# Kernel tuning notes

Hardware: AMD Instinct MI355X
Metric: run time of the kernel (lower is better)

The kernel has to match this reference:

```python
import jax, jax.numpy as jnp
import numpy as np

EPSILON = 1e-8
DAMPING = 0.7
B, PREV, SIZE, NXT = 8192, 2000, 2000, 2000


def standardize(x):
    # per-sample standardization over features (torch.std uses ddof=1)
    mean = x.mean(axis=1, keepdims=True)
    std = jnp.std(x, axis=1, ddof=1, keepdims=True)
    return (x - mean) / (std + EPSILON)


def setup_inputs() -> dict:
    key = jax.random.key(0)
    ks = jax.random.split(key, 9)
    return {
        "prev_act": jax.random.normal(ks[0], (B, PREV), jnp.float32),
        "self_act": jax.random.normal(ks[1], (B, SIZE), jnp.float32),
        "next_act": jax.random.normal(ks[2], (B, NXT), jnp.float32),
        "forward_W": jax.random.normal(ks[3], (SIZE, PREV), jnp.float32) * 0.02,
        "forward_b": jax.random.normal(ks[4], (SIZE,), jnp.float32) * 0.02,
        "backward_W": jax.random.normal(ks[5], (SIZE, NXT), jnp.float32) * 0.02,
        "backward_b": jax.random.normal(ks[6], (SIZE,), jnp.float32) * 0.02,
        "lateral_W": jax.random.normal(ks[7], (SIZE, SIZE), jnp.float32) * 0.02,
        "lateral_b": jax.random.normal(ks[8], (SIZE,), jnp.float32) * 0.02,
    }


def reference(prev_act, self_act, next_act, forward_W, forward_b,
              backward_W, backward_b, lateral_W, lateral_b):
    # middle HiddenLayer forward: fwd(prev) + next.backward(next) + lateral(self)
    prev_s = standardize(prev_act)   # [B, PREV]
    next_s = standardize(next_act)   # [B, NXT]
    self_s = standardize(self_act)   # [B, SIZE]
    pre = (jnp.einsum('bp,sp->bs', prev_s, forward_W) + forward_b
           + jnp.einsum('bn,sn->bs', next_s, backward_W) + backward_b
           + jnp.einsum('bk,sk->bs', self_s, lateral_W) + lateral_b)
    new_act = jax.nn.relu(pre)
    # damped recurrent update
    return DAMPING * new_act + (1.0 - DAMPING) * self_act
```

## Files before the change

kernel.cpp:

```cpp
#include <hip/hip_runtime.h>
#include <hip/hip_bf16.h>

constexpr int BATCH = 8192;
constexpr int NREAL = 2000;
constexpr int KSLOT = 2048;
constexpr int KPAD  = 6144;
constexpr int NPAD  = 2048;
constexpr int NT    = KPAD / 64;

typedef short bf16x8 __attribute__((ext_vector_type(8)));
typedef float f32x4  __attribute__((ext_vector_type(4)));

__device__ inline void gload_lds16(const void* g, void* l) {
  __builtin_amdgcn_global_load_lds(
      (const __attribute__((address_space(1))) unsigned int*)g,
      (__attribute__((address_space(3))) unsigned int*)l,
      16, 0, 0);
}

__device__ inline unsigned short f2bf(float x) {
  union { float f; unsigned int u; } v;
  v.f = x;
  unsigned int r = v.u + 0x7fffu + ((v.u >> 16) & 1u);
  return (unsigned short)(r >> 16);
}

__global__ __launch_bounds__(256) void pack_kernel(
    const float* __restrict__ prev, const float* __restrict__ nxt,
    const float* __restrict__ selfa,
    const float* __restrict__ fW, const float* __restrict__ bW,
    const float* __restrict__ lW,
    unsigned short* __restrict__ Acat, unsigned short* __restrict__ Wcat) {
  const int mat = blockIdx.y;
  const int t = threadIdx.x;

  if (blockIdx.x >= BATCH) {
    const int s = blockIdx.x - BATCH;
    uint4 q = make_uint4(0, 0, 0, 0);
    if (s < NREAL && t < 250) {
      const float* src = ((mat == 0) ? fW : (mat == 1) ? bW : lW) +
                         (size_t)s * NREAL + t * 8;
      const float4* p = (const float4*)src;
      float4 a = p[0], b = p[1];
      q.x = (unsigned)f2bf(a.x) | ((unsigned)f2bf(a.y) << 16);
      q.y = (unsigned)f2bf(a.z) | ((unsigned)f2bf(a.w) << 16);
      q.z = (unsigned)f2bf(b.x) | ((unsigned)f2bf(b.y) << 16);
      q.w = (unsigned)f2bf(b.z) | ((unsigned)f2bf(b.w) << 16);
    }
    *(uint4*)(Wcat + (size_t)s * KPAD + mat * KSLOT + t * 8) = q;
    return;
  }

  __shared__ float red[4];
  const int row = blockIdx.x;
  const float* src = (mat == 0) ? prev : (mat == 1) ? nxt : selfa;

  float x[8];
  float s1 = 0.f;
  if (t < 250) {
    const float4* p = (const float4*)(src + (size_t)row * NREAL + t * 8);
    float4 a = p[0], b = p[1];
    x[0] = a.x; x[1] = a.y; x[2] = a.z; x[3] = a.w;
    x[4] = b.x; x[5] = b.y; x[6] = b.z; x[7] = b.w;
#pragma unroll
    for (int j = 0; j < 8; ++j) s1 += x[j];
  } else {
#pragma unroll
    for (int j = 0; j < 8; ++j) x[j] = 0.f;
  }
#pragma unroll
  for (int o = 32; o; o >>= 1) s1 += __shfl_xor(s1, o);
  if ((t & 63) == 0) red[t >> 6] = s1;
  __syncthreads();
  const float mean = (red[0] + red[1] + red[2] + red[3]) * (1.f / 2000.f);
  __syncthreads();

  float ss = 0.f;
  if (t < 250) {
#pragma unroll
    for (int j = 0; j < 8; ++j) { float d = x[j] - mean; ss += d * d; }
  }
#pragma unroll
  for (int o = 32; o; o >>= 1) ss += __shfl_xor(ss, o);
  if ((t & 63) == 0) red[t >> 6] = ss;
  __syncthreads();
  const float var = (red[0] + red[1] + red[2] + red[3]) * (1.f / 1999.f);
  const float scale = 1.f / (sqrtf(var) + 1e-8f);

  unsigned short o8[8];
  if (t < 250) {
#pragma unroll
    for (int j = 0; j < 8; ++j) o8[j] = f2bf((x[j] - mean) * scale);
  } else {
#pragma unroll
    for (int j = 0; j < 8; ++j) o8[j] = 0;
  }
  uint4 q;
  q.x = (unsigned)o8[0] | ((unsigned)o8[1] << 16);
  q.y = (unsigned)o8[2] | ((unsigned)o8[3] << 16);
  q.z = (unsigned)o8[4] | ((unsigned)o8[5] << 16);
  q.w = (unsigned)o8[6] | ((unsigned)o8[7] << 16);
  *(uint4*)(Acat + (size_t)row * KPAD + mat * KSLOT + t * 8) = q;
}

__global__ __launch_bounds__(512, 2) void gemm_kernel(
    const unsigned short* __restrict__ A,
    const unsigned short* __restrict__ W,
    const float* __restrict__ fb, const float* __restrict__ bb,
    const float* __restrict__ lb,
    const float* __restrict__ selfact,
    float* __restrict__ out) {
  __shared__ unsigned short ldsS[2][2][2][256][32];
  unsigned short* ldsF = &ldsS[0][0][0][0][0];

  const int tid  = threadIdx.x;
  const int wave = tid >> 6;
  const int lane = tid & 63;
  const int wm = wave >> 2;
  const int wn = wave & 3;

  const int nbid = (blockIdx.x & 7) * 32 + (blockIdx.x >> 3);
  const int bm = nbid >> 3;
  const int bn = nbid & 7;

  const int srow = tid >> 2;
  const int sc = (tid & 3) ^ ((tid >> 3) & 3);
  const unsigned short* Asrc =
      A + (size_t)(bm * 256 + srow) * KPAD + sc * 8;
  const unsigned short* Bsrc =
      W + (size_t)(bn * 256 + srow) * KPAD + sc * 8;

  const int pcx = (lane >> 4) ^ ((lane >> 1) & 3);
  const unsigned short* aF = ldsF + (wm * 128 + (lane & 15)) * 32 + pcx * 8;
  const unsigned short* bF = ldsF + (wn * 64 + (lane & 15)) * 32 + pcx * 8;

  f32x4 acc[8][4] = {};
  bf16x8 bfr[4][2];

#define STQ(bu, mat, kq, rh, tt) { \
    const unsigned short* g_ = ((mat) ? Bsrc : Asrc) + \
        (size_t)(rh) * 128 * KPAD + (size_t)(tt) * 64 + (kq) * 32; \
    unsigned short* d_ = ldsF + ((bu) * 4 + (mat) * 2 + (kq)) * 8192 + \
        (rh) * 4096 + wave * 512; \
    gload_lds16(g_, d_); \
  }

#define READ_BF(bu) \
    _Pragma("unroll") for (int fn = 0; fn < 4; ++fn) \
    _Pragma("unroll") for (int kk = 0; kk < 2; ++kk) \
      bfr[fn][kk] = *(const bf16x8*)(bF + ((bu) * 4 + 2 + kk) * 8192 + fn * 512);

#define PHASE(bu, p, STG, GATE) { \
    bf16x8 a00 = *(const bf16x8*)(aF + ((bu) * 4 + 0) * 8192 + (2 * (p)) * 512); \
    bf16x8 a01 = *(const bf16x8*)(aF + ((bu) * 4 + 1) * 8192 + (2 * (p)) * 512); \
    bf16x8 a10 = *(const bf16x8*)(aF + ((bu) * 4 + 0) * 8192 + (2 * (p) + 1) * 512); \
    bf16x8 a11 = *(const bf16x8*)(aF + ((bu) * 4 + 1) * 8192 + (2 * (p) + 1) * 512); \
    if ((p) == 0) { READ_BF(bu) } \
    STG \
    if ((p) == 0) asm volatile("s_waitcnt lgkmcnt(8)" ::: "memory"); \
    __builtin_amdgcn_s_barrier(); \
    asm volatile("s_waitcnt lgkmcnt(0)" ::: "memory"); \
    __builtin_amdgcn_s_setprio(1); \
    _Pragma("unroll") for (int fn = 0; fn < 4; ++fn) { \
      acc[2 * (p)][fn] = __builtin_amdgcn_mfma_f32_16x16x32_bf16( \
          a00, bfr[fn][0], acc[2 * (p)][fn], 0, 0, 0); \
      acc[2 * (p)][fn] = __builtin_amdgcn_mfma_f32_16x16x32_bf16( \
          a01, bfr[fn][1], acc[2 * (p)][fn], 0, 0, 0); \
      acc[2 * (p) + 1][fn] = __builtin_amdgcn_mfma_f32_16x16x32_bf16( \
          a10, bfr[fn][0], acc[2 * (p) + 1][fn], 0, 0, 0); \
      acc[2 * (p) + 1][fn] = __builtin_amdgcn_mfma_f32_16x16x32_bf16( \
          a11, bfr[fn][1], acc[2 * (p) + 1][fn], 0, 0, 0); \
    } \
    __builtin_amdgcn_s_setprio(0); \
    GATE \
    __builtin_amdgcn_s_barrier(); \
  }

#define TILE(bu, t, SA, SB, GATE) { \
    PHASE(bu, 0, if (SA) { STQ((bu) ^ 1, 0, 0, 0, (t) + 1) STQ((bu) ^ 1, 0, 1, 0, (t) + 1) }, ) \
    PHASE(bu, 1, if (SA) { STQ((bu) ^ 1, 0, 0, 1, (t) + 1) STQ((bu) ^ 1, 0, 1, 1, (t) + 1) }, ) \
    PHASE(bu, 2, if (SB) { STQ((bu), 1, 0, 0, (t) + 2) STQ((bu), 1, 1, 0, (t) + 2) }, ) \
    PHASE(bu, 3, if (SB) { STQ((bu), 1, 0, 1, (t) + 2) STQ((bu), 1, 1, 1, (t) + 2) }, GATE) \
  }

  STQ(0, 0, 0, 0, 0) STQ(0, 0, 1, 0, 0)
  STQ(0, 0, 0, 1, 0) STQ(0, 0, 1, 1, 0)
  STQ(0, 1, 0, 0, 0) STQ(0, 1, 1, 0, 0)
  STQ(0, 1, 0, 1, 0) STQ(0, 1, 1, 1, 0)
  STQ(1, 1, 0, 0, 1) STQ(1, 1, 1, 0, 1)
  STQ(1, 1, 0, 1, 1) STQ(1, 1, 1, 1, 1)
  asm volatile("s_waitcnt vmcnt(4)" ::: "memory");
  __builtin_amdgcn_s_barrier();

  for (int i = 0; i < 47; ++i) {
    const int t = 2 * i;
    TILE(0, t, true, true,
         asm volatile("s_waitcnt vmcnt(4)" ::: "memory");)
    TILE(1, t + 1, true, true,
         asm volatile("s_waitcnt vmcnt(4)" ::: "memory");)
  }
  TILE(0, 94, true, false,
       asm volatile("s_waitcnt vmcnt(0)" ::: "memory");)
  TILE(1, 95, false, false, )

  const int colLane = lane & 15;
  const int rowGrp  = (lane >> 4) * 4;
#pragma unroll
  for (int fn = 0; fn < 4; ++fn) {
    const int col = bn * 256 + wn * 64 + fn * 16 + colLane;
    if (col < NREAL) {
      const float bias = fb[col] + bb[col] + lb[col];
#pragma unroll
      for (int fm = 0; fm < 8; ++fm) {
        const int row0 = bm * 256 + wm * 128 + fm * 16 + rowGrp;
#pragma unroll
        for (int r = 0; r < 4; ++r) {
          const float pre = acc[fm][fn][r] + bias;
          const size_t oi = (size_t)(row0 + r) * NREAL + col;
          out[oi] = 0.7f * fmaxf(pre, 0.f) + 0.3f * selfact[oi];
        }
      }
    }
  }
#undef TILE
#undef PHASE
#undef READ_BF
#undef STQ
}

extern "C" void kernel_launch(void* const* d_in, const int* in_sizes, int n_in,
                              void* d_out, int out_size, void* d_ws,
                              size_t ws_size, hipStream_t stream) {
  const float* prev = (const float*)d_in[0];
  const float* selfa = (const float*)d_in[1];
  const float* nxt  = (const float*)d_in[2];
  const float* fW = (const float*)d_in[3];
  const float* fb = (const float*)d_in[4];
  const float* bW = (const float*)d_in[5];
  const float* bb = (const float*)d_in[6];
  const float* lW = (const float*)d_in[7];
  const float* lb = (const float*)d_in[8];
  float* out = (float*)d_out;

  unsigned short* Acat = (unsigned short*)d_ws;
  unsigned short* Wcat = Acat + (size_t)BATCH * KPAD;

  pack_kernel<<<dim3(BATCH + NPAD, 3), 256, 0, stream>>>(
      prev, nxt, selfa, fW, bW, lW, Acat, Wcat);
  gemm_kernel<<<dim3(32 * 8), 512, 0, stream>>>(Acat, Wcat, fb, bb, lb,
                                                selfa, out);
}
```

Baseline: 255.5 us.

## Switch GEMM to 32x32x16 MFMA with simpler double-buffered tile loop

Replaces the 16x16x32 MFMA tiling with 32x32x16 MFMA, so each wave uses 4x2 accumulator blocks of 16 floats and fewer LDS fragment reads per FLOP. It also drops the finely phased four-stage pipeline with partial vmcnt gates. In its place is a plain loop that prefetches the whole next tile, computes the current one, then waits vmcnt(0) and hits a barrier once per tile. The larger MFMA should cut LDS traffic and instruction count, but the coarser synchronisation may expose more global-load latency.

```diff
diff --git a/kernel.cpp b/kernel.cpp
--- a/kernel.cpp
+++ b/kernel.cpp
@@ -9,7 +9,7 @@
 constexpr int NT    = KPAD / 64;
 
 typedef short bf16x8 __attribute__((ext_vector_type(8)));
-typedef float f32x4  __attribute__((ext_vector_type(4)));
+typedef float f32x16 __attribute__((ext_vector_type(16)));
 
 __device__ inline void gload_lds16(const void* g, void* l) {
   __builtin_amdgcn_global_load_lds(
@@ -130,12 +130,21 @@
   const unsigned short* Bsrc =
       W + (size_t)(bn * 256 + srow) * KPAD + sc * 8;
 
-  const int pcx = (lane >> 4) ^ ((lane >> 1) & 3);
-  const unsigned short* aF = ldsF + (wm * 128 + (lane & 15)) * 32 + pcx * 8;
-  const unsigned short* bF = ldsF + (wn * 64 + (lane & 15)) * 32 + pcx * 8;
-
-  f32x4 acc[8][4] = {};
-  bf16x8 bfr[4][2];
+  const int h = lane >> 5;
+  const int l31 = lane & 31;
+  int aOff[4], bOff[2];
+#pragma unroll
+  for (int rg = 0; rg < 4; ++rg) {
+    const int row = wm * 128 + rg * 32 + l31;
+    aOff[rg] = row * 32 + ((h ^ ((row >> 1) & 3)) << 3);
+  }
+#pragma unroll
+  for (int cg = 0; cg < 2; ++cg) {
+    const int row = wn * 64 + cg * 32 + l31;
+    bOff[cg] = row * 32 + ((h ^ ((row >> 1) & 3)) << 3);
+  }
+
+  f32x16 acc[4][2] = {};
 
 #define STQ(bu, mat, kq, rh, tt) { \
     const unsigned short* g_ = ((mat) ? Bsrc : Asrc) + \
@@ -144,87 +153,68 @@
         (rh) * 4096 + wave * 512; \
     gload_lds16(g_, d_); \
   }
-
-#define READ_BF(bu) \
-    _Pragma("unroll") for (int fn = 0; fn < 4; ++fn) \
-    _Pragma("unroll") for (int kk = 0; kk < 2; ++kk) \
-      bfr[fn][kk] = *(const bf16x8*)(bF + ((bu) * 4 + 2 + kk) * 8192 + fn * 512);
-
-#define PHASE(bu, p, STG, GATE) { \
-    bf16x8 a00 = *(const bf16x8*)(aF + ((bu) * 4 + 0) * 8192 + (2 * (p)) * 512); \
-    bf16x8 a01 = *(const bf16x8*)(aF + ((bu) * 4 + 1) * 8192 + (2 * (p)) * 512); \
-    bf16x8 a10 = *(const bf16x8*)(aF + ((bu) * 4 + 0) * 8192 + (2 * (p) + 1) * 512); \
-    bf16x8 a11 = *(const bf16x8*)(aF + ((bu) * 4 + 1) * 8192 + (2 * (p) + 1) * 512); \
-    if ((p) == 0) { READ_BF(bu) } \
-    STG \
-    if ((p) == 0) asm volatile("s_waitcnt lgkmcnt(8)" ::: "memory"); \
-    __builtin_amdgcn_s_barrier(); \
-    asm volatile("s_waitcnt lgkmcnt(0)" ::: "memory"); \
-    __builtin_amdgcn_s_setprio(1); \
-    _Pragma("unroll") for (int fn = 0; fn < 4; ++fn) { \
-      acc[2 * (p)][fn] = __builtin_amdgcn_mfma_f32_16x16x32_bf16( \
-          a00, bfr[fn][0], acc[2 * (p)][fn], 0, 0, 0); \
-      acc[2 * (p)][fn] = __builtin_amdgcn_mfma_f32_16x16x32_bf16( \
-          a01, bfr[fn][1], acc[2 * (p)][fn], 0, 0, 0); \
-      acc[2 * (p) + 1][fn] = __builtin_amdgcn_mfma_f32_16x16x32_bf16( \
-          a10, bfr[fn][0], acc[2 * (p) + 1][fn], 0, 0, 0); \
-      acc[2 * (p) + 1][fn] = __builtin_amdgcn_mfma_f32_16x16x32_bf16( \
-          a11, bfr[fn][1], acc[2 * (p) + 1][fn], 0, 0, 0); \
-    } \
-    __builtin_amdgcn_s_setprio(0); \
-    GATE \
-    __builtin_amdgcn_s_barrier(); \
-  }
-
-#define TILE(bu, t, SA, SB, GATE) { \
-    PHASE(bu, 0, if (SA) { STQ((bu) ^ 1, 0, 0, 0, (t) + 1) STQ((bu) ^ 1, 0, 1, 0, (t) + 1) }, ) \
-    PHASE(bu, 1, if (SA) { STQ((bu) ^ 1, 0, 0, 1, (t) + 1) STQ((bu) ^ 1, 0, 1, 1, (t) + 1) }, ) \
-    PHASE(bu, 2, if (SB) { STQ((bu), 1, 0, 0, (t) + 2) STQ((bu), 1, 1, 0, (t) + 2) }, ) \
-    PHASE(bu, 3, if (SB) { STQ((bu), 1, 0, 1, (t) + 2) STQ((bu), 1, 1, 1, (t) + 2) }, GATE) \
-  }
-
-  STQ(0, 0, 0, 0, 0) STQ(0, 0, 1, 0, 0)
-  STQ(0, 0, 0, 1, 0) STQ(0, 0, 1, 1, 0)
-  STQ(0, 1, 0, 0, 0) STQ(0, 1, 1, 0, 0)
-  STQ(0, 1, 0, 1, 0) STQ(0, 1, 1, 1, 0)
-  STQ(1, 1, 0, 0, 1) STQ(1, 1, 1, 0, 1)
-  STQ(1, 1, 0, 1, 1) STQ(1, 1, 1, 1, 1)
-  asm volatile("s_waitcnt vmcnt(4)" ::: "memory");
+#define STAGE_TILE(bu, tt) { \
+    STQ(bu, 0, 0, 0, tt) STQ(bu, 0, 1, 0, tt) \
+    STQ(bu, 0, 0, 1, tt) STQ(bu, 0, 1, 1, tt) \
+    STQ(bu, 1, 0, 0, tt) STQ(bu, 1, 1, 0, tt) \
+    STQ(bu, 1, 0, 1, tt) STQ(bu, 1, 1, 1, tt) }
+
+  STAGE_TILE(0, 0)
+  asm volatile("s_waitcnt vmcnt(0)" ::: "memory");
   __builtin_amdgcn_s_barrier();
-
-  for (int i = 0; i < 47; ++i) {
-    const int t = 2 * i;
-    TILE(0, t, true, true,
-         asm volatile("s_waitcnt vmcnt(4)" ::: "memory");)
-    TILE(1, t + 1, true, true,
-         asm volatile("s_waitcnt vmcnt(4)" ::: "memory");)
-  }
-  TILE(0, 94, true, false,
-       asm volatile("s_waitcnt vmcnt(0)" ::: "memory");)
-  TILE(1, 95, false, false, )
-
-  const int colLane = lane & 15;
-  const int rowGrp  = (lane >> 4) * 4;
-#pragma unroll
-  for (int fn = 0; fn < 4; ++fn) {
-    const int col = bn * 256 + wn * 64 + fn * 16 + colLane;
+  __builtin_amdgcn_sched_barrier(0);
+
+  for (int t = 0; t < NT; ++t) {
+    const int q = t & 1;
+    if (t + 1 < NT) STAGE_TILE(q ^ 1, t + 1)
+    const unsigned short* aB = ldsF + (q * 4 + 0) * 8192;
+    const unsigned short* bB = ldsF + (q * 4 + 2) * 8192;
+#pragma unroll
+    for (int kg = 0; kg < 4; ++kg) {
+      const int reg = (kg >> 1) * 8192;
+      const int kx = (kg & 1) << 4;
+      bf16x8 a0 = *(const bf16x8*)(aB + reg + (aOff[0] ^ kx));
+      bf16x8 a1 = *(const bf16x8*)(aB + reg + (aOff[1] ^ kx));
+      bf16x8 a2 = *(const bf16x8*)(aB + reg + (aOff[2] ^ kx));
+      bf16x8 a3 = *(const bf16x8*)(aB + reg + (aOff[3] ^ kx));
+      bf16x8 b0 = *(const bf16x8*)(bB + reg + (bOff[0] ^ kx));
+      bf16x8 b1 = *(const bf16x8*)(bB + reg + (bOff[1] ^ kx));
+      __builtin_amdgcn_s_setprio(1);
+      acc[0][0] = __builtin_amdgcn_mfma_f32_32x32x16_bf16(a0, b0, acc[0][0], 0, 0, 0);
+      acc[0][1] = __builtin_amdgcn_mfma_f32_32x32x16_bf16(a0, b1, acc[0][1], 0, 0, 0);
+      acc[1][0] = __builtin_amdgcn_mfma_f32_32x32x16_bf16(a1, b0, acc[1][0], 0, 0, 0);
+      acc[1][1] = __builtin_amdgcn_mfma_f32_32x32x16_bf16(a1, b1, acc[1][1], 0, 0, 0);
+      acc[2][0] = __builtin_amdgcn_mfma_f32_32x32x16_bf16(a2, b0, acc[2][0], 0, 0, 0);
+      acc[2][1] = __builtin_amdgcn_mfma_f32_32x32x16_bf16(a2, b1, acc[2][1], 0, 0, 0);
+      acc[3][0] = __builtin_amdgcn_mfma_f32_32x32x16_bf16(a3, b0, acc[3][0], 0, 0, 0);
+      acc[3][1] = __builtin_amdgcn_mfma_f32_32x32x16_bf16(a3, b1, acc[3][1], 0, 0, 0);
+      __builtin_amdgcn_s_setprio(0);
+    }
+    asm volatile("s_waitcnt vmcnt(0)" ::: "memory");
+    __builtin_amdgcn_s_barrier();
+    __builtin_amdgcn_sched_barrier(0);
+  }
+
+  const int colBase = bn * 256 + wn * 64 + l31;
+  const int rowBase = bm * 256 + wm * 128 + 4 * h;
+#pragma unroll
+  for (int cg = 0; cg < 2; ++cg) {
+    const int col = colBase + cg * 32;
     if (col < NREAL) {
       const float bias = fb[col] + bb[col] + lb[col];
 #pragma unroll
-      for (int fm = 0; fm < 8; ++fm) {
-        const int row0 = bm * 256 + wm * 128 + fm * 16 + rowGrp;
-#pragma unroll
-        for (int r = 0; r < 4; ++r) {
-          const float pre = acc[fm][fn][r] + bias;
-          const size_t oi = (size_t)(row0 + r) * NREAL + col;
+      for (int rg = 0; rg < 4; ++rg) {
+#pragma unroll
+        for (int r = 0; r < 16; ++r) {
+          const int row = rowBase + rg * 32 + (r & 3) + 8 * (r >> 2);
+          const size_t oi = (size_t)row * NREAL + col;
+          const float pre = acc[rg][cg][r] + bias;
           out[oi] = 0.7f * fmaxf(pre, 0.f) + 0.3f * selfact[oi];
         }
       }
     }
   }
-#undef TILE
-#undef PHASE
-#undef READ_BF
+#undef STAGE_TILE
 #undef STQ
 }
 
```

Result: slower. 266.8 us (+4.4%).
